# Performance work log

Measured on AMD Instinct MI355X. Metric: run time of the kernel, lower is better.

## Reference

```python
import jax, jax.numpy as jnp
import numpy as np
from math import factorial

# ---------- real-basis Wigner 3j (Clebsch-Gordan) constants ----------

def _su2_cg(j1, j2, j3, m1, m2, m3):
    if m3 != m1 + m2 or not (abs(j1 - j2) <= j3 <= j1 + j2):
        return 0.0
    f = factorial
    pref = ((2 * j3 + 1) * f(j3 + j1 - j2) * f(j3 - j1 + j2) * f(j1 + j2 - j3) / f(j1 + j2 + j3 + 1)) ** 0.5
    pref *= (f(j3 + m3) * f(j3 - m3) * f(j1 - m1) * f(j1 + m1) * f(j2 - m2) * f(j2 + m2)) ** 0.5
    s = 0.0
    for k in range(0, j1 + j2 - j3 + 1):
        args = [k, j1 + j2 - j3 - k, j1 - m1 - k, j2 + m2 - k, j3 - j2 + m1 + k, j3 - j1 - m2 + k]
        if any(a < 0 for a in args):
            continue
        d = 1.0
        for a in args:
            d *= f(a)
        s += (-1) ** k / d
    return pref * s


def _q(l):  # complex->real spherical harmonics change of basis (e3nn convention)
    q = np.zeros((2 * l + 1, 2 * l + 1), dtype=complex)
    for m in range(-l, 0):
        q[l + m, l + abs(m)] = 2 ** -0.5
        q[l + m, l - abs(m)] = -1j * 2 ** -0.5
    q[l, l] = 1.0
    for m in range(1, l + 1):
        q[l + m, l + abs(m)] = (-1) ** m * 2 ** -0.5
        q[l + m, l - abs(m)] = 1j * (-1) ** m * 2 ** -0.5
    return (-1j) ** l * q


def _wigner3j(l1, l2, l3):
    C = np.zeros((2 * l1 + 1, 2 * l2 + 1, 2 * l3 + 1))
    for m1 in range(-l1, l1 + 1):
        for m2 in range(-l2, l2 + 1):
            m3 = m1 + m2
            if -l3 <= m3 <= l3:
                C[l1 + m1, l2 + m2, l3 + m3] = _su2_cg(l1, l2, l3, m1, m2, m3)
    T = np.einsum('ai,bj,ck,ijk->abc', _q(l1), _q(l2), np.conj(_q(l3)), C)
    T = T.real if np.abs(T.real).sum() >= np.abs(T.imag).sum() else T.imag
    return (T / (2 * l3 + 1) ** 0.5).astype(np.float32)  # 3j normalization


LS = [0, 1, 2]                       # Rs_mid irreps (each multiplicity 1)
OFF = {0: (0, 1), 1: (1, 4), 2: (4, 9)}  # slices into the dim-9 irrep vector
L_OUT = [0, 1, 2, 3, 4]
MUL_OUT = {0: 64, 1: 64, 2: 64, 3: 32, 4: 16}
MUL_MID = 32
CG = {(l1, l2, l3): jnp.asarray(_wigner3j(l1, l2, l3))
      for l1 in LS for l2 in LS for l3 in range(abs(l1 - l2), l1 + l2 + 1)}


def setup_inputs():
    key = jax.random.key(0)
    ks = jax.random.split(key, 8)
    N = 50000
    x1 = jax.random.normal(ks[0], (N, MUL_MID * 9), jnp.float32)
    x2 = jax.random.normal(ks[1], (N, MUL_MID * 9), jnp.float32)
    n_paths = {l: 0 for l in L_OUT}
    for (_, _, l3) in CG:
        n_paths[l3] += 1
    out = {"x1": x1, "x2": x2}
    for i, l in enumerate(L_OUT):
        out[f"W{l}"] = jax.random.normal(ks[2 + i], (MUL_OUT[l], n_paths[l] * MUL_MID), jnp.float32)
    return out


def _forward(x1, x2, Ws):
    n = x1.shape[0]
    a = x1.reshape(n, MUL_MID, 9)
    b = x2.reshape(n, MUL_MID, 9)
    blocks = {l: [] for l in L_OUT}
    for l1 in LS:
        s1 = a[:, :, OFF[l1][0]:OFF[l1][1]]
        for l2 in LS:
            s2 = b[:, :, OFF[l2][0]:OFF[l2][1]]
            for l3 in range(abs(l1 - l2), l1 + l2 + 1):
                # [n, mul, 2l3+1] CG-gated bilinear contraction per channel
                blocks[l3].append(jnp.einsum('nui,nuj,ijk->nuk', s1, s2, CG[(l1, l2, l3)]))
    outs = []
    for l in L_OUT:
        feat = jnp.concatenate(blocks[l], axis=1)        # [n, mul_in, 2l+1]
        mul_in = feat.shape[1]
        o = jnp.einsum('nui,ou->noi', feat, Ws[l] / np.float32(np.sqrt(mul_in)))
        outs.append(o.reshape(n, -1))
    return jnp.concatenate(outs, axis=1)                 # [n, 944]


def reference(x1, x2, W0, W1, W2, W3, W4):
    return _forward(x1, x2, {0: W0, 1: W1, 2: W2, 3: W3, 4: W4})
```

## Files before the change

### kernel.cpp

```cpp
#include <hip/hip_runtime.h>
#include <hip/hip_fp16.h>
#include <array>

typedef __attribute__((ext_vector_type(8))) short short8;
typedef __attribute__((ext_vector_type(4))) float f32x4;
typedef __attribute__((ext_vector_type(4))) unsigned u32x4;

#define N_PATHS 19
#define SROW 148
#define HROW 290

constexpr int kPL1[N_PATHS]  = {0,0,0,1,1,1,1,1,1,1,2,2,2,2,2,2,2,2,2};
constexpr int kPL2[N_PATHS]  = {0,1,2,0,1,1,1,2,2,2,0,1,1,1,2,2,2,2,2};
constexpr int kPL3[N_PATHS]  = {0,1,2,1,0,1,2,1,2,3,2,1,2,3,0,1,2,3,4};
constexpr int kIOFF[3]  = {0,1,4};
constexpr int kSP[5][6] = {{0,4,14,0,0,0},{1,3,5,7,11,15},{2,6,8,10,12,16},{9,13,17,0,0,0},{18,0,0,0,0,0}};
constexpr int kKS[5] = {3,6,6,3,1};
constexpr int kNT[5] = {4,4,4,2,1};
constexpr int kOB[5] = {0,64,256,576,800};
constexpr int kFB[5] = {0,12,36,60,66};
#define N_FRAGS 67

struct ccplx { double re, im; };
constexpr ccplx cmulc(ccplx a, ccplx b){ return {a.re*b.re - a.im*b.im, a.re*b.im + a.im*b.re}; }
constexpr double cfact(int n){ double f = 1.0; for (int i = 2; i <= n; ++i) f *= i; return f; }
constexpr double csqrt(double x){
  if (x <= 0.0) return 0.0;
  double g = x > 1.0 ? x : 1.0;
  for (int i = 0; i < 64; ++i) g = 0.5*(g + x/g);
  return g;
}
constexpr double c_su2cg(int j1,int j2,int j3,int m1,int m2){
  int m3 = m1+m2;
  int am3 = m3 < 0 ? -m3 : m3;
  int dj = j1-j2 < 0 ? j2-j1 : j1-j2;
  if (j3 < dj || j3 > j1+j2 || am3 > j3) return 0.0;
  double pref = (2.0*j3+1.0)*cfact(j3+j1-j2)*cfact(j3-j1+j2)*cfact(j1+j2-j3)/cfact(j1+j2+j3+1);
  pref = csqrt(pref);
  pref *= csqrt(cfact(j3+m3)*cfact(j3-m3)*cfact(j1-m1)*cfact(j1+m1)*cfact(j2-m2)*cfact(j2+m2));
  double s = 0.0;
  for (int k = 0; k <= j1+j2-j3; ++k){
    int a1=j1+j2-j3-k, a2=j1-m1-k, a3=j2+m2-k, a4=j3-j2+m1+k, a5=j3-j1-m2+k;
    if (a1<0||a2<0||a3<0||a4<0||a5<0) continue;
    double d = cfact(k)*cfact(a1)*cfact(a2)*cfact(a3)*cfact(a4)*cfact(a5);
    s += ((k&1) ? -1.0 : 1.0)/d;
  }
  return pref*s;
}
constexpr ccplx qel(int l, int r, int c){
  const double rt = 0.70710678118654752440;
  int m = r - l;
  ccplx v{0.0, 0.0};
  if (m < 0){
    if (c == l - m) v = {rt, 0.0};
    else if (c == l + m) v = {0.0, -rt};
  } else if (m == 0){
    if (c == l) v = {1.0, 0.0};
  } else {
    double s = (m & 1) ? -1.0 : 1.0;
    if (c == l + m) v = {s*rt, 0.0};
    else if (c == l - m) v = {0.0, s*rt};
  }
  int ph = l & 3;
  if (ph == 1) return { v.im, -v.re};
  if (ph == 2) return {-v.re, -v.im};
  if (ph == 3) return {-v.im,  v.re};
  return v;
}
template<int P>
constexpr auto make_cg(){
  constexpr int l1 = kPL1[P], l2 = kPL2[P], l3 = kPL3[P];
  constexpr int D1 = 2*l1+1, D2v = 2*l2+1, D3 = 2*l3+1;
  double su[D1][D2v] = {};
  for (int i = 0; i < D1; ++i)
    for (int j = 0; j < D2v; ++j)
      su[i][j] = c_su2cg(l1, l2, l3, i-l1, j-l2);
  std::array<double, (size_t)D1*D2v*D3> re{}, im{};
  double sre = 0.0, sim = 0.0;
  for (int a = 0; a < D1; ++a)
    for (int b = 0; b < D2v; ++b)
      for (int c = 0; c < D3; ++c){
        ccplx acc{0.0, 0.0};
        for (int i = 0; i < D1; ++i)
          for (int j = 0; j < D2v; ++j){
            int kk = l3 + (i-l1) + (j-l2);
            if (kk < 0 || kk >= D3) continue;
            double cgv = su[i][j];
            if (cgv == 0.0) continue;
            ccplx q3 = qel(l3, c, kk);
            ccplx pr = cmulc(cmulc(qel(l1,a,i), qel(l2,b,j)), ccplx{q3.re, -q3.im});
            acc.re += pr.re*cgv; acc.im += pr.im*cgv;
          }
        size_t e = ((size_t)a*D2v + b)*D3 + c;
        re[e] = acc.re; im[e] = acc.im;
        sre += acc.re < 0 ? -acc.re : acc.re;
        sim += acc.im < 0 ? -acc.im : acc.im;
      }
  std::array<float, (size_t)D1*D2v*D3> out{};
  const bool useRe = (sre >= sim);
  const double norm = 1.0/csqrt((double)D3);
  for (size_t e = 0; e < out.size(); ++e){
    double v = (useRe ? re[e] : im[e])*norm;
    if (v < 1e-10 && v > -1e-10) v = 0.0;
    out[e] = (float)v;
  }
  return out;
}
template<int P> struct CGTab { static constexpr auto tab = make_cg<P>(); };
template<int P, int K> constexpr bool row_any(int E){
  for (int k = 0; k < K; ++k) if (CGTab<P>::tab[(size_t)E*K + k] != 0.0f) return true;
  return false;
}

__device__ inline unsigned short f2bf(float v){
  unsigned u = __builtin_bit_cast(unsigned, v);
  unsigned r = u + 0x7FFFu + ((u>>16)&1u);
  return (unsigned short)(r>>16);
}

__global__ void prep_w_kernel(const float* __restrict__ W0, const float* __restrict__ W1,
                              const float* __restrict__ W2, const float* __restrict__ W3,
                              const float* __restrict__ W4, unsigned short* __restrict__ wout){
  int el = blockIdx.x*256 + threadIdx.x;
  if (el >= N_FRAGS*512) return;
  int frag = el>>9, r = el&511, lam = r>>3, j = r&7;
  int l  = (frag<12)?0 : (frag<36)?1 : (frag<60)?2 : (frag<66)?3 : 4;
  int fb = (l==0)?0 : (l==1)?12 : (l==2)?36 : (l==3)?60 : 66;
  int Ks = (l==0)?3 : (l==1)?6 : (l==2)?6 : (l==3)?3 : 1;
  int U  = (l==0)?96 : (l==1)?192 : (l==2)?192 : (l==3)?96 : 32;
  int rel = frag - fb, nt = rel/Ks, tt = rel - nt*Ks;
  int o = nt*16 + (lam&15);
  int u = tt*32 + (lam>>4)*8 + j;
  const float* W = (l==0)?W0 : (l==1)?W1 : (l==2)?W2 : (l==3)?W3 : W4;
  float scale = (l==0||l==3) ? 0.10206207261596575f
              : (l==4)       ? 0.17677669529663687f
                             : 0.07216878364870323f;
  wout[el] = f2bf(W[o*U + u] * scale);
}


template<int P, int K, int E, int KK>
struct CKk {
  static __device__ __forceinline__ void run(float (&a0)[K], float (&a1)[K], float p0, float p1){
    constexpr float w = CGTab<P>::tab[(size_t)E*K + KK];
    if constexpr (w != 0.0f){
      a0[KK] = __builtin_fmaf(w, p0, a0[KK]);
      a1[KK] = __builtin_fmaf(w, p1, a1[KK]);
    }
    if constexpr (KK+1 < K) CKk<P,K,E,KK+1>::run(a0, a1, p0, p1);
  }
};

template<int P, int K, int D2v, int O1, int O2, int E, int NE>
struct CElem {
  static __device__ __forceinline__ void run(float (&a0)[K], float (&a1)[K],
                                             const float* xa, const float* xb){
    if constexpr (row_any<P,K>(E)){
      constexpr int i = E / D2v, jj = E - i*D2v;
      float p0 = xa[O1+i] * xb[O2+jj];
      float p1 = xa[9+O1+i] * xb[9+O2+jj];
      CKk<P,K,E,0>::run(a0, a1, p0, p1);
    }
    if constexpr (E+1 < NE) CElem<P,K,D2v,O1,O2,E+1,NE>::run(a0, a1, xa, xb);
  }
};

template<int L, int TT>
struct Slot {
  static constexpr int P  = kSP[L][TT];
  static constexpr int L1 = kPL1[P], L2_ = kPL2[P];
  static constexpr int D1 = 2*L1+1, D2v = 2*L2_+1;
  static constexpr int O1 = kIOFF[L1], O2 = kIOFF[L2_];
  static __device__ __forceinline__ void build(u32x4 (*af)[kKS[L]], const float* xa,
                                               const float* xb, int jp){
    constexpr int K = 2*L+1;
    float a0[K], a1[K];
    #pragma unroll
    for (int k=0;k<K;++k){ a0[k]=0.f; a1[k]=0.f; }
    CElem<P,K,D2v,O1,O2,0,D1*D2v>::run(a0, a1, xa, xb);
    #pragma unroll
    for (int k=0;k<K;++k){
      unsigned pk;
      asm("v_cvt_pk_bf16_f32 %0, %1, %2" : "=v"(pk) : "v"(a0[k]), "v"(a1[k]));
      af[k][TT][jp] = pk;
    }
    if constexpr (TT+1 < kKS[L]) Slot<L, TT+1>::build(af, xa, xb, jp);
  }
};

template<int L>
__device__ __forceinline__ void do_group(const __half* __restrict__ i1p,
                                         const __half* __restrict__ i2p,
                                         const short* __restrict__ wfrag,
                                         float* slab, float* __restrict__ out,
                                         int nrowb, int N, int lane){
  constexpr int K = 2*L+1, Ks = kKS[L], Nt = kNT[L];
  const int s = lane&15, g = lane>>4;
  u32x4 af[K][Ks];

  #pragma unroll
  for (int jp=0; jp<4; ++jp){
    float xa[18], xb[18];
    #pragma unroll
    for (int e=0; e<9; ++e){
      __half2 va = *reinterpret_cast<const __half2*>(i1p + jp*18 + e*2);
      __half2 vb = *reinterpret_cast<const __half2*>(i2p + jp*18 + e*2);
      xa[e*2] = __half2float(va.x); xa[e*2+1] = __half2float(va.y);
      xb[e*2] = __half2float(vb.x); xb[e*2+1] = __half2float(vb.y);
    }
    Slot<L,0>::build(af, xa, xb, jp);
  }

  const short* wf = wfrag + (size_t)kFB[L]*512 + (size_t)lane*8;
  short8 bfc[Ks], bfn[Ks];
  #pragma unroll
  for (int tt=0; tt<Ks; ++tt)
    bfc[tt] = *reinterpret_cast<const short8*>(wf + tt*512);
  #pragma unroll
  for (int nt=0; nt<Nt; ++nt){
    if (nt+1 < Nt){
      #pragma unroll
      for (int tt=0; tt<Ks; ++tt)
        bfn[tt] = *reinterpret_cast<const short8*>(wf + ((nt+1)*Ks+tt)*512);
    }
    f32x4 acc[K];
    #pragma unroll
    for (int k=0;k<K;++k) acc[k] = (f32x4){0.f,0.f,0.f,0.f};
    #pragma unroll
    for (int tt=0; tt<Ks; ++tt)
      #pragma unroll
      for (int k=0;k<K;++k)
        acc[k] = __builtin_amdgcn_mfma_f32_16x16x32_bf16(
                   __builtin_bit_cast(short8, af[k][tt]), bfc[tt], acc[k], 0, 0, 0);
    #pragma unroll
    for (int k=0;k<K;++k)
      #pragma unroll
      for (int r=0;r<4;++r)
        slab[(g*4+r)*SROW + s*K + k] = acc[k][r];
    const int rr = lane>>2, q4 = lane&3;
    const float* sp = slab + rr*SROW;
    const bool on = (nrowb + rr) < N;
    float* op = out + (size_t)(nrowb+rr)*944 + kOB[L] + nt*16*K;
    #pragma unroll
    for (int c=0;c<K;++c){
      float4 v = *reinterpret_cast<const float4*>(sp + (c*4+q4)*4);
      if (on) *reinterpret_cast<float4*>(op + (c*4+q4)*4) = v;
    }
    if (nt+1 < Nt){
      #pragma unroll
      for (int tt=0; tt<Ks; ++tt) bfc[tt] = bfn[tt];
    }
  }
}

__global__ __launch_bounds__(128, 2) void tp_main(
    const float* __restrict__ x1, const float* __restrict__ x2,
    const short* __restrict__ wfrag, float* __restrict__ out, int N)
{
  __shared__ __align__(16) __half in1h[16*HROW];
  __shared__ __align__(16) __half in2h[16*HROW];
  __shared__ __align__(16) float stage[2*16*SROW];
  const int t = threadIdx.x, w = t>>6, lane = t&63;
  const int nb = blockIdx.x*16;

  for (int idx = t; idx < 16*72; idx += 128){
    int row = idx/72, c4 = idx - row*72;
    int n = nb + row;
    float4 v1 = {0,0,0,0}, v2 = {0,0,0,0};
    if (n < N){
      v1 = reinterpret_cast<const float4*>(x1 + (size_t)n*288)[c4];
      v2 = reinterpret_cast<const float4*>(x2 + (size_t)n*288)[c4];
    }
    int b = row*HROW + c4*4;
    ushort4 u1, u2;
    u1.x = __half_as_ushort(__float2half_rn(v1.x)); u1.y = __half_as_ushort(__float2half_rn(v1.y));
    u1.z = __half_as_ushort(__float2half_rn(v1.z)); u1.w = __half_as_ushort(__float2half_rn(v1.w));
    u2.x = __half_as_ushort(__float2half_rn(v2.x)); u2.y = __half_as_ushort(__float2half_rn(v2.y));
    u2.z = __half_as_ushort(__float2half_rn(v2.z)); u2.w = __half_as_ushort(__float2half_rn(v2.w));
    *reinterpret_cast<ushort4*>(&in1h[b]) = u1;
    *reinterpret_cast<ushort4*>(&in2h[b]) = u2;
  }
  __syncthreads();

  const int s = lane&15, g = lane>>4;
  const __half* i1p = &in1h[s*HROW + g*72];
  const __half* i2p = &in2h[s*HROW + g*72];
  float* slab = &stage[w*16*SROW];

  if (w == 0){
    do_group<0>(i1p, i2p, wfrag, slab, out, nb, N, lane);
    do_group<1>(i1p, i2p, wfrag, slab, out, nb, N, lane);
    do_group<3>(i1p, i2p, wfrag, slab, out, nb, N, lane);
  } else {
    do_group<2>(i1p, i2p, wfrag, slab, out, nb, N, lane);
    do_group<4>(i1p, i2p, wfrag, slab, out, nb, N, lane);
  }
}

extern "C" void kernel_launch(void* const* d_in, const int* in_sizes, int n_in,
                              void* d_out, int out_size, void* d_ws, size_t ws_size,
                              hipStream_t stream)
{
  (void)n_in; (void)out_size; (void)ws_size;
  const float* x1 = (const float*)d_in[0];
  const float* x2 = (const float*)d_in[1];
  const float* W0 = (const float*)d_in[2];
  const float* W1 = (const float*)d_in[3];
  const float* W2 = (const float*)d_in[4];
  const float* W3 = (const float*)d_in[5];
  const float* W4 = (const float*)d_in[6];
  float* out = (float*)d_out;
  int N = in_sizes[0] / 288;

  prep_w_kernel<<<dim3((N_FRAGS*512 + 255)/256), dim3(256), 0, stream>>>(
      W0, W1, W2, W3, W4, (unsigned short*)d_ws);
  int grid = (N + 15) / 16;
  tp_main<<<dim3(grid), dim3(128), 0, stream>>>(
      x1, x2, (const short*)d_ws, out, N);
}
```

Measured before the change: 110.4 us.

## Read inputs directly from global memory instead of fp16 LDS staging

Drops the cooperative global-to-LDS staging of x1/x2, which converted them to fp16 and needed a block barrier. Each lane now reads its row's float2 pairs straight from global memory, relying on L1/L2 to absorb the repeated reads across groups. With the LDS input buffers gone, launch bounds rise to 4 blocks per CU for more occupancy. The trade-off is that the same input rows are re-read from global memory by each do_group call and by both waves, using strided, poorly coalesced accesses, and register pressure is capped more tightly.

```diff
diff --git a/kernel.cpp b/kernel.cpp
--- a/kernel.cpp
+++ b/kernel.cpp
@@ -1,5 +1,4 @@
 #include <hip/hip_runtime.h>
-#include <hip/hip_fp16.h>
 #include <array>
 
 typedef __attribute__((ext_vector_type(8))) short short8;
@@ -8,7 +7,6 @@
 
 #define N_PATHS 19
 #define SROW 148
-#define HROW 290
 
 constexpr int kPL1[N_PATHS]  = {0,0,0,1,1,1,1,1,1,1,2,2,2,2,2,2,2,2,2};
 constexpr int kPL2[N_PATHS]  = {0,1,2,0,1,1,1,2,2,2,0,1,1,1,2,2,2,2,2};
@@ -189,8 +187,8 @@
 };
 
 template<int L>
-__device__ __forceinline__ void do_group(const __half* __restrict__ i1p,
-                                         const __half* __restrict__ i2p,
+__device__ __forceinline__ void do_group(const float* __restrict__ x1g,
+                                         const float* __restrict__ x2g, bool act,
                                          const short* __restrict__ wfrag,
                                          float* slab, float* __restrict__ out,
                                          int nrowb, int N, int lane){
@@ -203,10 +201,13 @@
     float xa[18], xb[18];
     #pragma unroll
     for (int e=0; e<9; ++e){
-      __half2 va = *reinterpret_cast<const __half2*>(i1p + jp*18 + e*2);
-      __half2 vb = *reinterpret_cast<const __half2*>(i2p + jp*18 + e*2);
-      xa[e*2] = __half2float(va.x); xa[e*2+1] = __half2float(va.y);
-      xb[e*2] = __half2float(vb.x); xb[e*2+1] = __half2float(vb.y);
+      float2 va = {0.f,0.f}, vb = {0.f,0.f};
+      if (act){
+        va = *reinterpret_cast<const float2*>(x1g + jp*18 + e*2);
+        vb = *reinterpret_cast<const float2*>(x2g + jp*18 + e*2);
+      }
+      xa[e*2] = va.x; xa[e*2+1] = va.y;
+      xb[e*2] = vb.x; xb[e*2+1] = vb.y;
     }
     Slot<L,0>::build(af, xa, xb, jp);
   }
@@ -253,47 +254,28 @@
   }
 }
 
-__global__ __launch_bounds__(128, 2) void tp_main(
+__global__ __launch_bounds__(128, 4) void tp_main(
     const float* __restrict__ x1, const float* __restrict__ x2,
     const short* __restrict__ wfrag, float* __restrict__ out, int N)
 {
-  __shared__ __align__(16) __half in1h[16*HROW];
-  __shared__ __align__(16) __half in2h[16*HROW];
   __shared__ __align__(16) float stage[2*16*SROW];
   const int t = threadIdx.x, w = t>>6, lane = t&63;
   const int nb = blockIdx.x*16;
-
-  for (int idx = t; idx < 16*72; idx += 128){
-    int row = idx/72, c4 = idx - row*72;
-    int n = nb + row;
-    float4 v1 = {0,0,0,0}, v2 = {0,0,0,0};
-    if (n < N){
-      v1 = reinterpret_cast<const float4*>(x1 + (size_t)n*288)[c4];
-      v2 = reinterpret_cast<const float4*>(x2 + (size_t)n*288)[c4];
-    }
-    int b = row*HROW + c4*4;
-    ushort4 u1, u2;
-    u1.x = __half_as_ushort(__float2half_rn(v1.x)); u1.y = __half_as_ushort(__float2half_rn(v1.y));
-    u1.z = __half_as_ushort(__float2half_rn(v1.z)); u1.w = __half_as_ushort(__float2half_rn(v1.w));
-    u2.x = __half_as_ushort(__float2half_rn(v2.x)); u2.y = __half_as_ushort(__float2half_rn(v2.y));
-    u2.z = __half_as_ushort(__float2half_rn(v2.z)); u2.w = __half_as_ushort(__float2half_rn(v2.w));
-    *reinterpret_cast<ushort4*>(&in1h[b]) = u1;
-    *reinterpret_cast<ushort4*>(&in2h[b]) = u2;
-  }
-  __syncthreads();
-
   const int s = lane&15, g = lane>>4;
-  const __half* i1p = &in1h[s*HROW + g*72];
-  const __half* i2p = &in2h[s*HROW + g*72];
+  const int n = nb + s;
+  const bool act = n < N;
+  const size_t nbeg = (size_t)(act ? n : 0)*288 + g*72;
+  const float* x1g = x1 + nbeg;
+  const float* x2g = x2 + nbeg;
   float* slab = &stage[w*16*SROW];
 
   if (w == 0){
-    do_group<0>(i1p, i2p, wfrag, slab, out, nb, N, lane);
-    do_group<1>(i1p, i2p, wfrag, slab, out, nb, N, lane);
-    do_group<3>(i1p, i2p, wfrag, slab, out, nb, N, lane);
+    do_group<0>(x1g, x2g, act, wfrag, slab, out, nb, N, lane);
+    do_group<1>(x1g, x2g, act, wfrag, slab, out, nb, N, lane);
+    do_group<3>(x1g, x2g, act, wfrag, slab, out, nb, N, lane);
   } else {
-    do_group<2>(i1p, i2p, wfrag, slab, out, nb, N, lane);
-    do_group<4>(i1p, i2p, wfrag, slab, out, nb, N, lane);
+    do_group<2>(x1g, x2g, act, wfrag, slab, out, nb, N, lane);
+    do_group<4>(x1g, x2g, act, wfrag, slab, out, nb, N, lane);
   }
 }
 
```

Result: slower. 411.3 us (+272.5%).

## Interleave per-path A-fragment build with MFMA and store accumulators directly

Applied to the files above, without the earlier changes.

Restructures each output group so the A fragments are built one path slot at a time and consumed immediately by MFMAs into per-n-tile accumulators held across all slots. Only the needed input spans are loaded for each path. The LDS staging slab is removed and accumulators are written straight to global memory as scalar stores. Occupancy in launch_bounds rises from 2 to 3. The aim is lower register pressure and less LDS traffic, at the cost of scattered, uncoalesced scalar global stores and repeated LDS input reads for every path slot.

```diff
diff --git a/kernel.cpp b/kernel.cpp
--- a/kernel.cpp
+++ b/kernel.cpp
@@ -7,7 +7,6 @@
 typedef __attribute__((ext_vector_type(4))) unsigned u32x4;
 
 #define N_PATHS 19
-#define SROW 148
 #define HROW 290
 
 constexpr int kPL1[N_PATHS]  = {0,0,0,1,1,1,1,1,1,1,2,2,2,2,2,2,2,2,2};
@@ -165,26 +164,56 @@
   }
 };
 
+template<int O, int D>
+__device__ __forceinline__ void load_span(float* x, const __half* p){
+  #pragma unroll
+  for (int h = (O & ~1); h < O + D; h += 2){
+    __half2 v = *reinterpret_cast<const __half2*>(p + h);
+    x[h] = __half2float(v.x); x[h+1] = __half2float(v.y);
+  }
+  #pragma unroll
+  for (int h = ((9+O) & ~1); h < 9 + O + D; h += 2){
+    __half2 v = *reinterpret_cast<const __half2*>(p + h);
+    x[h] = __half2float(v.x); x[h+1] = __half2float(v.y);
+  }
+}
+
 template<int L, int TT>
-struct Slot {
+struct TT2 {
   static constexpr int P  = kSP[L][TT];
   static constexpr int L1 = kPL1[P], L2_ = kPL2[P];
   static constexpr int D1 = 2*L1+1, D2v = 2*L2_+1;
   static constexpr int O1 = kIOFF[L1], O2 = kIOFF[L2_];
-  static __device__ __forceinline__ void build(u32x4 (*af)[kKS[L]], const float* xa,
-                                               const float* xb, int jp){
-    constexpr int K = 2*L+1;
-    float a0[K], a1[K];
+  static constexpr int K = 2*L+1, Ks = kKS[L], Nt = kNT[L];
+  static __device__ __forceinline__ void run(f32x4 (&acc)[kNT[L]][2*L+1],
+                                             const __half* i1p, const __half* i2p,
+                                             const short* wf){
+    u32x4 af[K];
     #pragma unroll
-    for (int k=0;k<K;++k){ a0[k]=0.f; a1[k]=0.f; }
-    CElem<P,K,D2v,O1,O2,0,D1*D2v>::run(a0, a1, xa, xb);
+    for (int jp=0; jp<4; ++jp){
+      float xa[18], xb[18];
+      load_span<O1,D1>(xa, i1p + jp*18);
+      load_span<O2,D2v>(xb, i2p + jp*18);
+      float a0[K], a1[K];
+      #pragma unroll
+      for (int k=0;k<K;++k){ a0[k]=0.f; a1[k]=0.f; }
+      CElem<P,K,D2v,O1,O2,0,D1*D2v>::run(a0, a1, xa, xb);
+      #pragma unroll
+      for (int k=0;k<K;++k){
+        unsigned pk;
+        asm("v_cvt_pk_bf16_f32 %0, %1, %2" : "=v"(pk) : "v"(a0[k]), "v"(a1[k]));
+        af[k][jp] = pk;
+      }
+    }
     #pragma unroll
-    for (int k=0;k<K;++k){
-      unsigned pk;
-      asm("v_cvt_pk_bf16_f32 %0, %1, %2" : "=v"(pk) : "v"(a0[k]), "v"(a1[k]));
-      af[k][TT][jp] = pk;
-    }
-    if constexpr (TT+1 < kKS[L]) Slot<L, TT+1>::build(af, xa, xb, jp);
+    for (int nt=0; nt<Nt; ++nt){
+      const short8 bf = *reinterpret_cast<const short8*>(wf + (nt*Ks+TT)*512);
+      #pragma unroll
+      for (int k=0;k<K;++k)
+        acc[nt][k] = __builtin_amdgcn_mfma_f32_16x16x32_bf16(
+                       __builtin_bit_cast(short8, af[k]), bf, acc[nt][k], 0, 0, 0);
+    }
+    if constexpr (TT+1 < Ks) TT2<L,TT+1>::run(acc, i1p, i2p, wf);
   }
 };
 
@@ -192,74 +221,39 @@
 __device__ __forceinline__ void do_group(const __half* __restrict__ i1p,
                                          const __half* __restrict__ i2p,
                                          const short* __restrict__ wfrag,
-                                         float* slab, float* __restrict__ out,
+                                         float* __restrict__ out,
                                          int nrowb, int N, int lane){
-  constexpr int K = 2*L+1, Ks = kKS[L], Nt = kNT[L];
+  constexpr int K = 2*L+1, Nt = kNT[L];
   const int s = lane&15, g = lane>>4;
-  u32x4 af[K][Ks];
-
+  f32x4 acc[Nt][K];
   #pragma unroll
-  for (int jp=0; jp<4; ++jp){
-    float xa[18], xb[18];
+  for (int nt=0;nt<Nt;++nt)
     #pragma unroll
-    for (int e=0; e<9; ++e){
-      __half2 va = *reinterpret_cast<const __half2*>(i1p + jp*18 + e*2);
-      __half2 vb = *reinterpret_cast<const __half2*>(i2p + jp*18 + e*2);
-      xa[e*2] = __half2float(va.x); xa[e*2+1] = __half2float(va.y);
-      xb[e*2] = __half2float(vb.x); xb[e*2+1] = __half2float(vb.y);
-    }
-    Slot<L,0>::build(af, xa, xb, jp);
-  }
+    for (int k=0;k<K;++k) acc[nt][k] = (f32x4){0.f,0.f,0.f,0.f};
 
   const short* wf = wfrag + (size_t)kFB[L]*512 + (size_t)lane*8;
-  short8 bfc[Ks], bfn[Ks];
+  TT2<L,0>::run(acc, i1p, i2p, wf);
+
   #pragma unroll
-  for (int tt=0; tt<Ks; ++tt)
-    bfc[tt] = *reinterpret_cast<const short8*>(wf + tt*512);
-  #pragma unroll
-  for (int nt=0; nt<Nt; ++nt){
-    if (nt+1 < Nt){
+  for (int r=0;r<4;++r){
+    const int n = nrowb + g*4 + r;
+    if (n < N){
+      float* op = out + (size_t)n*944 + kOB[L] + s*K;
       #pragma unroll
-      for (int tt=0; tt<Ks; ++tt)
-        bfn[tt] = *reinterpret_cast<const short8*>(wf + ((nt+1)*Ks+tt)*512);
-    }
-    f32x4 acc[K];
-    #pragma unroll
-    for (int k=0;k<K;++k) acc[k] = (f32x4){0.f,0.f,0.f,0.f};
-    #pragma unroll
-    for (int tt=0; tt<Ks; ++tt)
-      #pragma unroll
-      for (int k=0;k<K;++k)
-        acc[k] = __builtin_amdgcn_mfma_f32_16x16x32_bf16(
-                   __builtin_bit_cast(short8, af[k][tt]), bfc[tt], acc[k], 0, 0, 0);
-    #pragma unroll
-    for (int k=0;k<K;++k)
-      #pragma unroll
-      for (int r=0;r<4;++r)
-        slab[(g*4+r)*SROW + s*K + k] = acc[k][r];
-    const int rr = lane>>2, q4 = lane&3;
-    const float* sp = slab + rr*SROW;
-    const bool on = (nrowb + rr) < N;
-    float* op = out + (size_t)(nrowb+rr)*944 + kOB[L] + nt*16*K;
-    #pragma unroll
-    for (int c=0;c<K;++c){
-      float4 v = *reinterpret_cast<const float4*>(sp + (c*4+q4)*4);
-      if (on) *reinterpret_cast<float4*>(op + (c*4+q4)*4) = v;
-    }
-    if (nt+1 < Nt){
-      #pragma unroll
-      for (int tt=0; tt<Ks; ++tt) bfc[tt] = bfn[tt];
-    }
-  }
-}
-
-__global__ __launch_bounds__(128, 2) void tp_main(
+      for (int nt=0;nt<Nt;++nt)
+        #pragma unroll
+        for (int k=0;k<K;++k)
+          op[nt*16*K + k] = acc[nt][k][r];
+    }
+  }
+}
+
+__global__ __launch_bounds__(128, 3) void tp_main(
     const float* __restrict__ x1, const float* __restrict__ x2,
     const short* __restrict__ wfrag, float* __restrict__ out, int N)
 {
   __shared__ __align__(16) __half in1h[16*HROW];
   __shared__ __align__(16) __half in2h[16*HROW];
-  __shared__ __align__(16) float stage[2*16*SROW];
   const int t = threadIdx.x, w = t>>6, lane = t&63;
   const int nb = blockIdx.x*16;
 
@@ -285,15 +279,14 @@
   const int s = lane&15, g = lane>>4;
   const __half* i1p = &in1h[s*HROW + g*72];
   const __half* i2p = &in2h[s*HROW + g*72];
-  float* slab = &stage[w*16*SROW];
 
   if (w == 0){
-    do_group<0>(i1p, i2p, wfrag, slab, out, nb, N, lane);
-    do_group<1>(i1p, i2p, wfrag, slab, out, nb, N, lane);
-    do_group<3>(i1p, i2p, wfrag, slab, out, nb, N, lane);
+    do_group<0>(i1p, i2p, wfrag, out, nb, N, lane);
+    do_group<1>(i1p, i2p, wfrag, out, nb, N, lane);
+    do_group<3>(i1p, i2p, wfrag, out, nb, N, lane);
   } else {
-    do_group<2>(i1p, i2p, wfrag, slab, out, nb, N, lane);
-    do_group<4>(i1p, i2p, wfrag, slab, out, nb, N, lane);
+    do_group<2>(i1p, i2p, wfrag, out, nb, N, lane);
+    do_group<4>(i1p, i2p, wfrag, out, nb, N, lane);
   }
 }
 
```

After: 380.5 us. 3.45x slower.

## Switch CG products to packed fp16 math and fp16 MFMA with transposed LDS layout

Applied to the files above, without the earlier changes.

Replaces the fp32 per-element CG contraction and bf16 conversion with packed half2 multiply/FMA, processing two channels per instruction, and switches the MFMA to the f16 variant with fp16 weights. The shared-memory input layout is transposed to component-major per 8-channel group so half2 pairs load directly. The MFMA loop is reordered to accumulate all output tiles per path slot, building A fragments per slot instead of holding them all. This reduces ALU work and register pressure, at the cost of fp16 accumulation of CG sums (range/precision risk), scalar 2-byte LDS stores during staging, and more live accumulators.

```diff
diff --git a/kernel.cpp b/kernel.cpp
--- a/kernel.cpp
+++ b/kernel.cpp
@@ -2,13 +2,13 @@
 #include <hip/hip_fp16.h>
 #include <array>
 
-typedef __attribute__((ext_vector_type(8))) short short8;
+typedef __attribute__((ext_vector_type(8))) _Float16 f16x8;
 typedef __attribute__((ext_vector_type(4))) float f32x4;
 typedef __attribute__((ext_vector_type(4))) unsigned u32x4;
 
 #define N_PATHS 19
 #define SROW 148
-#define HROW 290
+#define SROWH 298
 
 constexpr int kPL1[N_PATHS]  = {0,0,0,1,1,1,1,1,1,1,2,2,2,2,2,2,2,2,2};
 constexpr int kPL2[N_PATHS]  = {0,1,2,0,1,1,1,2,2,2,0,1,1,1,2,2,2,2,2};
@@ -111,11 +111,21 @@
   for (int k = 0; k < K; ++k) if (CGTab<P>::tab[(size_t)E*K + k] != 0.0f) return true;
   return false;
 }
-
-__device__ inline unsigned short f2bf(float v){
-  unsigned u = __builtin_bit_cast(unsigned, v);
-  unsigned r = u + 0x7FFFu + ((u>>16)&1u);
-  return (unsigned short)(r>>16);
+constexpr unsigned short h_bits(double v){
+  if (v == 0.0) return 0;
+  unsigned short s = 0;
+  if (v < 0){ s = 0x8000; v = -v; }
+  int e = 0;
+  while (v >= 2.0){ v *= 0.5; ++e; }
+  while (v < 1.0){ v *= 2.0; --e; }
+  double m = (v - 1.0) * 1024.0;
+  int mi = (int)(m + 0.5);
+  if (mi == 1024){ mi = 0; ++e; }
+  return (unsigned short)(s | ((unsigned)(e + 15) << 10) | (unsigned)mi);
+}
+constexpr unsigned h2_bits(double v){
+  unsigned short h = h_bits(v);
+  return (unsigned)h | ((unsigned)h << 16);
 }
 
 __global__ void prep_w_kernel(const float* __restrict__ W0, const float* __restrict__ W1,
@@ -135,56 +145,71 @@
   float scale = (l==0||l==3) ? 0.10206207261596575f
               : (l==4)       ? 0.17677669529663687f
                              : 0.07216878364870323f;
-  wout[el] = f2bf(W[o*U + u] * scale);
+  wout[el] = __half_as_ushort(__float2half_rn(W[o*U + u] * scale));
 }
 
 
 template<int P, int K, int E, int KK>
-struct CKk {
-  static __device__ __forceinline__ void run(float (&a0)[K], float (&a1)[K], float p0, float p1){
+struct PKk {
+  static __device__ __forceinline__ void run(__half2 (&a)[K], __half2 p){
     constexpr float w = CGTab<P>::tab[(size_t)E*K + KK];
     if constexpr (w != 0.0f){
-      a0[KK] = __builtin_fmaf(w, p0, a0[KK]);
-      a1[KK] = __builtin_fmaf(w, p1, a1[KK]);
-    }
-    if constexpr (KK+1 < K) CKk<P,K,E,KK+1>::run(a0, a1, p0, p1);
+      constexpr unsigned W2 = h2_bits((double)w);
+      a[KK] = __hfma2(__builtin_bit_cast(__half2, W2), p, a[KK]);
+    }
+    if constexpr (KK+1 < K) PKk<P,K,E,KK+1>::run(a, p);
   }
 };
 
-template<int P, int K, int D2v, int O1, int O2, int E, int NE>
-struct CElem {
-  static __device__ __forceinline__ void run(float (&a0)[K], float (&a1)[K],
-                                             const float* xa, const float* xb){
+template<int P, int K, int D2v, int E, int NE>
+struct PElem {
+  static __device__ __forceinline__ void run(__half2 (&a)[K],
+                                             const __half2* xa, const __half2* xb){
     if constexpr (row_any<P,K>(E)){
       constexpr int i = E / D2v, jj = E - i*D2v;
-      float p0 = xa[O1+i] * xb[O2+jj];
-      float p1 = xa[9+O1+i] * xb[9+O2+jj];
-      CKk<P,K,E,0>::run(a0, a1, p0, p1);
-    }
-    if constexpr (E+1 < NE) CElem<P,K,D2v,O1,O2,E+1,NE>::run(a0, a1, xa, xb);
+      __half2 p = __hmul2(xa[i], xb[jj]);
+      PKk<P,K,E,0>::run(a, p);
+    }
+    if constexpr (E+1 < NE) PElem<P,K,D2v,E+1,NE>::run(a, xa, xb);
   }
 };
 
 template<int L, int TT>
-struct Slot {
+struct TTF {
   static constexpr int P  = kSP[L][TT];
   static constexpr int L1 = kPL1[P], L2_ = kPL2[P];
   static constexpr int D1 = 2*L1+1, D2v = 2*L2_+1;
   static constexpr int O1 = kIOFF[L1], O2 = kIOFF[L2_];
-  static __device__ __forceinline__ void build(u32x4 (*af)[kKS[L]], const float* xa,
-                                               const float* xb, int jp){
-    constexpr int K = 2*L+1;
-    float a0[K], a1[K];
-    #pragma unroll
-    for (int k=0;k<K;++k){ a0[k]=0.f; a1[k]=0.f; }
-    CElem<P,K,D2v,O1,O2,0,D1*D2v>::run(a0, a1, xa, xb);
-    #pragma unroll
-    for (int k=0;k<K;++k){
-      unsigned pk;
-      asm("v_cvt_pk_bf16_f32 %0, %1, %2" : "=v"(pk) : "v"(a0[k]), "v"(a1[k]));
-      af[k][TT][jp] = pk;
-    }
-    if constexpr (TT+1 < kKS[L]) Slot<L, TT+1>::build(af, xa, xb, jp);
+  static constexpr int K = 2*L+1, Ks = kKS[L], Nt = kNT[L];
+  static __device__ __forceinline__ void run(f32x4 (&acc)[kNT[L]][2*L+1],
+                                             const __half* i1p, const __half* i2p,
+                                             const short* wf){
+    u32x4 af[K];
+    #pragma unroll
+    for (int jp=0; jp<4; ++jp){
+      __half2 xa[D1], xb[D2v];
+      #pragma unroll
+      for (int i=0;i<D1;++i)
+        xa[i] = *reinterpret_cast<const __half2*>(i1p + (O1+i)*8 + jp*2);
+      #pragma unroll
+      for (int j=0;j<D2v;++j)
+        xb[j] = *reinterpret_cast<const __half2*>(i2p + (O2+j)*8 + jp*2);
+      __half2 a[K];
+      #pragma unroll
+      for (int k=0;k<K;++k) a[k] = __builtin_bit_cast(__half2, 0u);
+      PElem<P,K,D2v,0,D1*D2v>::run(a, xa, xb);
+      #pragma unroll
+      for (int k=0;k<K;++k) af[k][jp] = __builtin_bit_cast(unsigned, a[k]);
+    }
+    #pragma unroll
+    for (int nt=0; nt<Nt; ++nt){
+      const f16x8 bf = *reinterpret_cast<const f16x8*>(wf + (nt*Ks+TT)*512);
+      #pragma unroll
+      for (int k=0;k<K;++k)
+        acc[nt][k] = __builtin_amdgcn_mfma_f32_16x16x32_f16(
+                       __builtin_bit_cast(f16x8, af[k]), bf, acc[nt][k], 0, 0, 0);
+    }
+    if constexpr (TT+1 < Ks) TTF<L,TT+1>::run(acc, i1p, i2p, wf);
   }
 };
 
@@ -194,49 +219,24 @@
                                          const short* __restrict__ wfrag,
                                          float* slab, float* __restrict__ out,
                                          int nrowb, int N, int lane){
-  constexpr int K = 2*L+1, Ks = kKS[L], Nt = kNT[L];
+  constexpr int K = 2*L+1, Nt = kNT[L];
   const int s = lane&15, g = lane>>4;
-  u32x4 af[K][Ks];
-
+  f32x4 acc[Nt][K];
   #pragma unroll
-  for (int jp=0; jp<4; ++jp){
-    float xa[18], xb[18];
-    #pragma unroll
-    for (int e=0; e<9; ++e){
-      __half2 va = *reinterpret_cast<const __half2*>(i1p + jp*18 + e*2);
-      __half2 vb = *reinterpret_cast<const __half2*>(i2p + jp*18 + e*2);
-      xa[e*2] = __half2float(va.x); xa[e*2+1] = __half2float(va.y);
-      xb[e*2] = __half2float(vb.x); xb[e*2+1] = __half2float(vb.y);
-    }
-    Slot<L,0>::build(af, xa, xb, jp);
-  }
+  for (int nt=0;nt<Nt;++nt)
+    #pragma unroll
+    for (int k=0;k<K;++k) acc[nt][k] = (f32x4){0.f,0.f,0.f,0.f};
 
   const short* wf = wfrag + (size_t)kFB[L]*512 + (size_t)lane*8;
-  short8 bfc[Ks], bfn[Ks];
-  #pragma unroll
-  for (int tt=0; tt<Ks; ++tt)
-    bfc[tt] = *reinterpret_cast<const short8*>(wf + tt*512);
+  TTF<L,0>::run(acc, i1p, i2p, wf);
+
   #pragma unroll
   for (int nt=0; nt<Nt; ++nt){
-    if (nt+1 < Nt){
-      #pragma unroll
-      for (int tt=0; tt<Ks; ++tt)
-        bfn[tt] = *reinterpret_cast<const short8*>(wf + ((nt+1)*Ks+tt)*512);
-    }
-    f32x4 acc[K];
-    #pragma unroll
-    for (int k=0;k<K;++k) acc[k] = (f32x4){0.f,0.f,0.f,0.f};
-    #pragma unroll
-    for (int tt=0; tt<Ks; ++tt)
-      #pragma unroll
-      for (int k=0;k<K;++k)
-        acc[k] = __builtin_amdgcn_mfma_f32_16x16x32_bf16(
-                   __builtin_bit_cast(short8, af[k][tt]), bfc[tt], acc[k], 0, 0, 0);
     #pragma unroll
     for (int k=0;k<K;++k)
       #pragma unroll
       for (int r=0;r<4;++r)
-        slab[(g*4+r)*SROW + s*K + k] = acc[k][r];
+        slab[(g*4+r)*SROW + s*K + k] = acc[nt][k][r];
     const int rr = lane>>2, q4 = lane&3;
     const float* sp = slab + rr*SROW;
     const bool on = (nrowb + rr) < N;
@@ -246,10 +246,6 @@
       float4 v = *reinterpret_cast<const float4*>(sp + (c*4+q4)*4);
       if (on) *reinterpret_cast<float4*>(op + (c*4+q4)*4) = v;
     }
-    if (nt+1 < Nt){
-      #pragma unroll
-      for (int tt=0; tt<Ks; ++tt) bfc[tt] = bfn[tt];
-    }
   }
 }
 
@@ -257,8 +253,8 @@
     const float* __restrict__ x1, const float* __restrict__ x2,
     const short* __restrict__ wfrag, float* __restrict__ out, int N)
 {
-  __shared__ __align__(16) __half in1h[16*HROW];
-  __shared__ __align__(16) __half in2h[16*HROW];
+  __shared__ __align__(16) __half in1h[16*SROWH];
+  __shared__ __align__(16) __half in2h[16*SROWH];
   __shared__ __align__(16) float stage[2*16*SROW];
   const int t = threadIdx.x, w = t>>6, lane = t&63;
   const int nb = blockIdx.x*16;
@@ -271,20 +267,23 @@
       v1 = reinterpret_cast<const float4*>(x1 + (size_t)n*288)[c4];
       v2 = reinterpret_cast<const float4*>(x2 + (size_t)n*288)[c4];
     }
-    int b = row*HROW + c4*4;
-    ushort4 u1, u2;
-    u1.x = __half_as_ushort(__float2half_rn(v1.x)); u1.y = __half_as_ushort(__float2half_rn(v1.y));
-    u1.z = __half_as_ushort(__float2half_rn(v1.z)); u1.w = __half_as_ushort(__float2half_rn(v1.w));
-    u2.x = __half_as_ushort(__float2half_rn(v2.x)); u2.y = __half_as_ushort(__float2half_rn(v2.y));
-    u2.z = __half_as_ushort(__float2half_rn(v2.z)); u2.w = __half_as_ushort(__float2half_rn(v2.w));
-    *reinterpret_cast<ushort4*>(&in1h[b]) = u1;
-    *reinterpret_cast<ushort4*>(&in2h[b]) = u2;
+    float a1v[4] = {v1.x, v1.y, v1.z, v1.w};
+    float a2v[4] = {v2.x, v2.y, v2.z, v2.w};
+    #pragma unroll
+    for (int u=0; u<4; ++u){
+      int c = c4*4 + u;
+      int m = c/9, e = c - m*9;
+      int g = m>>3, j = m&7;
+      int haddr = row*SROWH + g*72 + e*8 + j;
+      in1h[haddr] = __float2half_rn(a1v[u]);
+      in2h[haddr] = __float2half_rn(a2v[u]);
+    }
   }
   __syncthreads();
 
   const int s = lane&15, g = lane>>4;
-  const __half* i1p = &in1h[s*HROW + g*72];
-  const __half* i2p = &in2h[s*HROW + g*72];
+  const __half* i1p = &in1h[s*SROWH + g*72];
+  const __half* i2p = &in2h[s*SROWH + g*72];
   float* slab = &stage[w*16*SROW];
 
   if (w == 0){
```

After: 89.31 us. -19.1%, faster.
